# Kernel tuning notes

Hardware: AMD Instinct MI355X
Metric: run time of the kernel (lower is better)

Reference implementation:

```python
import jax, jax.numpy as jnp
import numpy as np

H = 16            # num_heads
D = 64            # head_output_size
DIM = 1024        # model dim (C)
R = 10            # lora rank
ATT_SCALE = D ** -0.5
LORA_SCALE = 1.0 / R   # lora_alpha(=1) / r


def setup_inputs() -> dict:
    key = jax.random.key(0)
    ks = jax.random.split(key, 14)
    B, N = 2, 2048
    s = 0.02
    x = jax.random.normal(ks[0], (B, N, DIM), jnp.float32)
    mask = jax.random.randint(ks[1], (B, N), 0, 2).astype(bool)
    return {
        "x": x,
        "mask": mask,
        "w_qkv": jax.random.normal(ks[2], (3 * H * D, DIM), jnp.float32) * s,
        "wq_base": jax.random.normal(ks[3], (H * D, DIM), jnp.float32) * s,
        "bq_base": jax.random.normal(ks[4], (H * D,), jnp.float32) * s,
        "wq_A": jax.random.normal(ks[5], (R, DIM), jnp.float32) * s,
        "wq_B": jax.random.normal(ks[6], (H * D, R), jnp.float32) * s,
        "wv_base": jax.random.normal(ks[7], (H * D, DIM), jnp.float32) * s,
        "bv_base": jax.random.normal(ks[8], (H * D,), jnp.float32) * s,
        "wv_A": jax.random.normal(ks[9], (R, DIM), jnp.float32) * s,
        "wv_B": jax.random.normal(ks[10], (H * D, R), jnp.float32) * s,
        "w_out": jax.random.normal(ks[11], (DIM, H * D), jnp.float32) * s,
        "b_out": jax.random.normal(ks[12], (DIM,), jnp.float32) * s,
    }


def _lora_linear(x, w_base, b_base, A, Bm):
    # lora.Linear (unmerged): base linear + scaled low-rank path
    return x @ w_base.T + b_base + ((x @ A.T) @ Bm.T) * LORA_SCALE


def reference(x, mask, w_qkv, wq_base, bq_base, wq_A, wq_B,
              wv_base, bv_base, wv_A, wv_B, w_out, b_out):
    B, N, C = x.shape
    # fused qkv projection -> (3, B, H, N, D)
    qkv = (x @ w_qkv.T).reshape(B, N, 3, H, D).transpose(2, 0, 3, 1, 4)
    q, k, v = qkv[0], qkv[1], qkv[2]
    # LoRA-modified q and v, reshaped to (B, H, N, D)
    q_lora = _lora_linear(x, wq_base, bq_base, wq_A, wq_B).reshape(B, N, H, D).transpose(0, 2, 1, 3)
    v_lora = _lora_linear(x, wv_base, bv_base, wv_A, wv_B).reshape(B, N, H, D).transpose(0, 2, 1, 3)
    q = q + q_lora
    v = v + v_lora
    # attention scores (B, H, N, N)
    attn = jnp.einsum('bhnd,bhmd->bhnm', q, k) * ATT_SCALE
    # 2D key-padding mask branch: mask[:, None, None, :]
    attn = jnp.where(mask[:, None, None, :], attn, -jnp.inf)
    attn = jax.nn.softmax(attn, axis=-1)
    out = jnp.einsum('bhnm,bhmd->bhnd', attn, v)
    out = out.transpose(0, 2, 1, 3).reshape(B, N, H * D)  # b h n d -> b n (h d)
    return out @ w_out.T + b_out
```

## Files before the change

kernel.cpp:

```cpp
#include <hip/hip_runtime.h>

typedef unsigned short u16;
typedef unsigned int u32;
typedef __attribute__((ext_vector_type(2))) unsigned int u32x2;
typedef __attribute__((ext_vector_type(4))) unsigned int u32x4;
typedef __attribute__((ext_vector_type(4))) unsigned short u16x4;
typedef __attribute__((ext_vector_type(8))) unsigned short u16x8;
typedef __attribute__((ext_vector_type(8))) short short8;
typedef __attribute__((ext_vector_type(4))) float f32x4;
typedef __attribute__((ext_vector_type(16))) float f32x16;

#define NHEAD 16
#define HDIM 64
#define SEQ 2048
#define MODELD 1024
#define MROWS 4096
#define QKVCOLS 3072
#define QSCALE 0.18033688011112042f

#define WAITVM(N) asm volatile("s_waitcnt vmcnt(" #N ")" ::: "memory")

__device__ __forceinline__ u16 f2bf(float f) {
  union { float f; unsigned u; } v; v.f = f;
  unsigned r = v.u + 0x7FFFu + ((v.u >> 16) & 1u);
  return (u16)(r >> 16);
}

__device__ __forceinline__ u32 cvtpk(float lo, float hi) {
  u32 r;
  asm("v_cvt_pk_bf16_f32 %0, %1, %2" : "=v"(r) : "v"(lo), "v"(hi));
  return r;
}

__device__ __forceinline__ void pl32(u32& a, u32& b) {
  asm("v_permlane32_swap_b32 %0, %1" : "+v"(a), "+v"(b));
}

__device__ __forceinline__ void gload_lds16(const void* g, void* l) {
  __builtin_amdgcn_global_load_lds((const __attribute__((address_space(1))) void*)g,
                                   (__attribute__((address_space(3))) void*)l, 16, 0, 0);
}


__global__ void prep_cast(const float* __restrict__ in, u16* __restrict__ outb) {
  int i = blockIdx.x * 256 + threadIdx.x;
  float4 v = *(const float4*)(in + (size_t)i * 4);
  u16x4 o = {f2bf(v.x), f2bf(v.y), f2bf(v.z), f2bf(v.w)};
  *(u16x4*)(outb + (size_t)i * 4) = o;
}

__global__ void prep_mask(const unsigned int* __restrict__ mraw, float* __restrict__ mf) {
  __shared__ int flag;
  const int tid = threadIdx.x;
  if (tid == 0) flag = 0;
  __syncthreads();
  if (mraw[tid] > 1u) flag = 1;
  __syncthreads();
  const int is_bytes = flag;
  const unsigned char* bp = (const unsigned char*)mraw;
#pragma unroll
  for (int j = 0; j < 4; ++j) {
    unsigned v = is_bytes ? (unsigned)bp[tid * 4 + j] : mraw[tid * 4 + j];
    mf[tid * 4 + j] = v ? 0.f : -1e30f;
  }
}

__global__ void prep_w(const float* __restrict__ wqkv,
                       const float* __restrict__ wqb, const float* __restrict__ bq,
                       const float* __restrict__ wqA, const float* __restrict__ wqB,
                       const float* __restrict__ wvb, const float* __restrict__ bv,
                       const float* __restrict__ wvA, const float* __restrict__ wvB,
                       u16* __restrict__ wcomb, float* __restrict__ biasc) {
  const int c = blockIdx.x;
  const int t = c >> 10, hd = c & 1023;
  const int k0 = threadIdx.x * 4;
  float4 w = *(const float4*)(wqkv + (size_t)c * MODELD + k0);
  float a0 = w.x, a1 = w.y, a2 = w.z, a3 = w.w;
  if (t != 1) {
    const float* base = (t == 0 ? wqb : wvb) + (size_t)hd * MODELD + k0;
    const float* A = (t == 0 ? wqA : wvA);
    const float* Bm = (t == 0 ? wqB : wvB) + hd * 10;
    float4 bsv = *(const float4*)base;
    a0 += bsv.x; a1 += bsv.y; a2 += bsv.z; a3 += bsv.w;
#pragma unroll
    for (int j = 0; j < 10; ++j) {
      float bj = Bm[j] * 0.1f;
      float4 av = *(const float4*)(A + (size_t)j * MODELD + k0);
      a0 += bj * av.x; a1 += bj * av.y; a2 += bj * av.z; a3 += bj * av.w;
    }
    if (t == 0) { a0 *= QSCALE; a1 *= QSCALE; a2 *= QSCALE; a3 *= QSCALE; }
  }
  u16x4 o = {f2bf(a0), f2bf(a1), f2bf(a2), f2bf(a3)};
  *(u16x4*)(wcomb + (size_t)c * MODELD + k0) = o;
  if (threadIdx.x == 0)
    biasc[c] = (t == 0) ? QSCALE * bq[hd] : ((t == 2) ? bv[hd] : 0.f);
}

template<int MODE>
__global__ __launch_bounds__(256) void gemm128(const u16* __restrict__ A, const u16* __restrict__ W,
                                               const float* __restrict__ bias,
                                               u16* __restrict__ oq, u16* __restrict__ ok, u16* __restrict__ ov,
                                               float* __restrict__ of) {
  __shared__ __align__(16) char lds[32768];
  const int tid = threadIdx.x;
  const int lane = tid & 63;
  const int wid = tid >> 6;
  const int wr = wid >> 1, wc = wid & 1;
  const int m0 = blockIdx.y << 7;
  const int n0 = blockIdx.x << 7;
  const int K = MODELD;

  f32x4 acc[4][4] = {};

  const int so = wid * 1024 + (lane << 4);
  for (int kt = 0; kt < K; kt += 64) {
#pragma unroll
    for (int c = 0; c < 4; ++c) {
      const int o = c * 4096 + so;
      const int row = o >> 7;
      const int colb = (o & 127) ^ ((row & 7) << 4);
      gload_lds16((const char*)(A + (size_t)(m0 + row) * K + kt) + colb, lds + (c * 4096 + wid * 1024));
      gload_lds16((const char*)(W + (size_t)(n0 + row) * K + kt) + colb, lds + (16384 + c * 4096 + wid * 1024));
    }
    __syncthreads();
#pragma unroll
    for (int ks = 0; ks < 2; ++ks) {
      short8 av[4], bv[4];
#pragma unroll
      for (int i = 0; i < 4; ++i) {
        const int arow = wr * 64 + i * 16 + (lane & 15);
        const int off = (ks * 64 + ((lane >> 4) << 4)) ^ ((lane & 7) << 4);
        av[i] = *(const short8*)(lds + (arow << 7) + off);
        const int brow = wc * 64 + i * 16 + (lane & 15);
        bv[i] = *(const short8*)(lds + 16384 + (brow << 7) + off);
      }
#pragma unroll
      for (int i = 0; i < 4; ++i)
#pragma unroll
        for (int j = 0; j < 4; ++j)
          acc[i][j] = __builtin_amdgcn_mfma_f32_16x16x32_bf16(av[i], bv[j], acc[i][j], 0, 0, 0);
    }
    __syncthreads();
  }

  if (MODE == 0) {
#pragma unroll
    for (int j = 0; j < 4; ++j) {
      const int col = n0 + wc * 64 + j * 16 + (lane & 15);
      const int tsel = col >> 10;
      const int hd = col & 1023;
      const int hh = hd >> 6, d = hd & 63;
      const float bs = bias[col];
#pragma unroll
      for (int i = 0; i < 4; ++i) {
        const int rowb = m0 + wr * 64 + i * 16 + ((lane >> 4) << 2);
#pragma unroll
        for (int r = 0; r < 4; ++r) {
          const int row = rowb + r;
          const int b = row >> 11, kv = row & 2047;
          const int bh = b * NHEAD + hh;
          const u16 val = f2bf(acc[i][j][r] + bs);
          if (tsel == 0) {
            oq[((size_t)bh * SEQ + kv) * HDIM + d] = val;
          } else if (tsel == 1) {
            ok[((size_t)(bh * 32 + (kv >> 6))) * 4096 +
               (size_t)(((((kv >> 5) & 1) << 2) + (d >> 4)) * 512) +
               (size_t)((((kv & 31) + (((d >> 3) & 1) << 5)) << 3) + (d & 7))] = val;
          } else {
            ov[((size_t)(bh * 32 + (kv >> 6))) * 4096 +
               (size_t)((((d >> 5) << 2) + ((kv >> 4) & 3)) * 512) +
               (size_t)((((d & 31) + (((kv >> 3) & 1) << 5)) << 3) + (kv & 7))] = val;
          }
        }
      }
    }
  } else {
#pragma unroll
    for (int j = 0; j < 4; ++j) {
      const int col = n0 + wc * 64 + j * 16 + (lane & 15);
      const float bs = bias[col];
#pragma unroll
      for (int i = 0; i < 4; ++i) {
        const int rowb = m0 + wr * 64 + i * 16 + ((lane >> 4) << 2);
#pragma unroll
        for (int r = 0; r < 4; ++r)
          of[(size_t)(rowb + r) * MODELD + col] = acc[i][j][r] + bs;
      }
    }
  }
}

__global__ __launch_bounds__(256) void flash_attn(const u16* __restrict__ q, const u16* __restrict__ kfr,
                                                  const u16* __restrict__ vfr, const float* __restrict__ maskf,
                                                  u16* __restrict__ attnout) {
  __shared__ __align__(16) char lds[73728];
  const int tid = threadIdx.x;
  const int lane = tid & 63, wid = tid >> 6;
  const int qi = lane & 31, h = lane >> 5;
  const int bid = blockIdx.x;
  const int bh = (bid & 7) * 4 + (bid >> 7);
  const int q0 = ((bid >> 3) & 15) * 128;
  const int b = bh >> 4, hh = bh & 15;

  const int token = q0 + wid * 32 + qi;
  short8 qf[4];
  {
    const u16* qp = q + ((size_t)bh * SEQ + token) * HDIM;
#pragma unroll
    for (int ks = 0; ks < 4; ++ks) qf[ks] = *(const short8*)(qp + ks * 16 + h * 8);
  }

  {
    const char* ms = (const char*)(maskf + b * SEQ);
    gload_lds16(ms + tid * 16, lds + 65536 + tid * 16);
    gload_lds16(ms + 4096 + tid * 16, lds + 65536 + 4096 + tid * 16);
  }

  const int so = tid << 4;
  const char* kg = (const char*)kfr + ((size_t)bh * 32) * 8192;
  const char* vg = (const char*)vfr + ((size_t)bh * 32) * 8192;
  auto stage = [&](int t) {
    char* kd = lds + ((t & 3) << 14);
    const char* ks = kg + (size_t)t * 8192;
    const char* vs = vg + (size_t)t * 8192;
    gload_lds16(ks + so, kd + so);
    gload_lds16(ks + 4096 + so, kd + 4096 + so);
    gload_lds16(vs + so, kd + 8192 + so);
    gload_lds16(vs + 4096 + so, kd + 12288 + so);
  };
  stage(0); stage(1); stage(2);

  f32x16 o0 = {}, o1 = {};
  f32x4 ps = {0.f, 0.f, 0.f, 0.f};

  for (int t = 0; t < 32; ++t) {
    if (t < 30)      { WAITVM(8); }
    else if (t == 30){ WAITVM(4); }
    else             { WAITVM(0); }
    asm volatile("s_barrier" ::: "memory");
    if (t <= 28) stage(t + 3);

    char* kb = lds + ((t & 3) << 14);
    char* vb = kb + 8192;
    const char* mrow = lds + 65536 + (t << 8);

    f32x16 s0 = {}, s1 = {};
    __builtin_amdgcn_s_setprio(1);
#pragma unroll
    for (int ks = 0; ks < 4; ++ks) {
      short8 ak0 = *(const short8*)(kb + (ks << 10) + (lane << 4));
      short8 ak1 = *(const short8*)(kb + 4096 + (ks << 10) + (lane << 4));
      s0 = __builtin_amdgcn_mfma_f32_32x32x16_bf16(ak0, qf[ks], s0, 0, 0, 0);
      s1 = __builtin_amdgcn_mfma_f32_32x32x16_bf16(ak1, qf[ks], s1, 0, 0, 0);
    }
    __builtin_amdgcn_s_setprio(0);

    u32 w[16];
#pragma unroll
    for (int blk = 0; blk < 2; ++blk) {
#pragma unroll
      for (int g = 0; g < 4; ++g) {
        f32x4 mk = *(const f32x4*)(mrow + blk * 128 + (g << 5) + (h << 4));
        float e0, e1, e2, e3;
        if (blk == 0) {
          e0 = exp2f(s0[4 * g + 0] + mk[0]); e1 = exp2f(s0[4 * g + 1] + mk[1]);
          e2 = exp2f(s0[4 * g + 2] + mk[2]); e3 = exp2f(s0[4 * g + 3] + mk[3]);
        } else {
          e0 = exp2f(s1[4 * g + 0] + mk[0]); e1 = exp2f(s1[4 * g + 1] + mk[1]);
          e2 = exp2f(s1[4 * g + 2] + mk[2]); e3 = exp2f(s1[4 * g + 3] + mk[3]);
        }
        ps[0] += e0; ps[1] += e1; ps[2] += e2; ps[3] += e3;
        w[blk * 8 + 2 * g] = cvtpk(e0, e1);
        w[blk * 8 + 2 * g + 1] = cvtpk(e2, e3);
      }
    }
    pl32(w[0], w[2]);  pl32(w[1], w[3]);
    pl32(w[4], w[6]);  pl32(w[5], w[7]);
    pl32(w[8], w[10]); pl32(w[9], w[11]);
    pl32(w[12], w[14]); pl32(w[13], w[15]);

    __builtin_amdgcn_s_setprio(1);
#pragma unroll
    for (int s = 0; s < 4; ++s) {
      u32x4 pw = {w[4 * s], w[4 * s + 1], w[4 * s + 2], w[4 * s + 3]};
      short8 pf = __builtin_bit_cast(short8, pw);
      short8 av0 = *(const short8*)(vb + (s << 10) + (lane << 4));
      short8 av1 = *(const short8*)(vb + 4096 + (s << 10) + (lane << 4));
      o0 = __builtin_amdgcn_mfma_f32_32x32x16_bf16(av0, pf, o0, 0, 0, 0);
      o1 = __builtin_amdgcn_mfma_f32_32x32x16_bf16(av1, pf, o1, 0, 0, 0);
    }
    __builtin_amdgcn_s_setprio(0);
  }

  float l = (ps[0] + ps[1]) + (ps[2] + ps[3]);
  l += __shfl_xor(l, 32);
  const float inv = 1.0f / l;

  u16* outp = attnout + ((size_t)(b * SEQ + token)) * MODELD + hh * HDIM;
#pragma unroll
  for (int dblk = 0; dblk < 2; ++dblk) {
#pragma unroll
    for (int g = 0; g < 4; ++g) {
      float v0, v1, v2, v3;
      if (dblk == 0) {
        v0 = o0[4 * g + 0]; v1 = o0[4 * g + 1]; v2 = o0[4 * g + 2]; v3 = o0[4 * g + 3];
      } else {
        v0 = o1[4 * g + 0]; v1 = o1[4 * g + 1]; v2 = o1[4 * g + 2]; v3 = o1[4 * g + 3];
      }
      u32x2 ow;
      ow[0] = cvtpk(v0 * inv, v1 * inv);
      ow[1] = cvtpk(v2 * inv, v3 * inv);
      *(u32x2*)(outp + dblk * 32 + g * 8 + h * 4) = ow;
    }
  }
}

extern "C" void kernel_launch(void* const* d_in, const int* in_sizes, int n_in,
                              void* d_out, int out_size, void* d_ws, size_t ws_size,
                              hipStream_t stream) {
  const float* x       = (const float*)d_in[0];
  const unsigned int* mask = (const unsigned int*)d_in[1];
  const float* w_qkv   = (const float*)d_in[2];
  const float* wq_base = (const float*)d_in[3];
  const float* bq      = (const float*)d_in[4];
  const float* wq_A    = (const float*)d_in[5];
  const float* wq_B    = (const float*)d_in[6];
  const float* wv_base = (const float*)d_in[7];
  const float* bv      = (const float*)d_in[8];
  const float* wv_A    = (const float*)d_in[9];
  const float* wv_B    = (const float*)d_in[10];
  const float* w_out   = (const float*)d_in[11];
  const float* b_out   = (const float*)d_in[12];
  float* out = (float*)d_out;

  char* ws = (char*)d_ws;
  u16* xb      = (u16*)(ws);
  u16* wcomb   = (u16*)(ws + 8388608);
  u16* woutb   = (u16*)(ws + 14680064);
  u16* qws     = (u16*)(ws + 16777216);
  u16* kws     = (u16*)(ws + 25165824);
  u16* vws     = (u16*)(ws + 33554432);
  float* biasc = (float*)(ws + 50331648);
  float* maskf = (float*)(ws + 50343936);
  u16* attnout = xb;

  prep_cast<<<4096, 256, 0, stream>>>(x, xb);
  prep_cast<<<1024, 256, 0, stream>>>(w_out, woutb);
  prep_mask<<<1, 1024, 0, stream>>>(mask, maskf);
  prep_w<<<3072, 256, 0, stream>>>(w_qkv, wq_base, bq, wq_A, wq_B,
                                   wv_base, bv, wv_A, wv_B, wcomb, biasc);

  gemm128<0><<<dim3(QKVCOLS / 128, MROWS / 128), 256, 0, stream>>>(
      xb, wcomb, biasc, qws, kws, vws, nullptr);

  flash_attn<<<512, 256, 0, stream>>>(qws, kws, vws, maskf, attnout);

  gemm128<1><<<dim3(MODELD / 128, MROWS / 128), 256, 0, stream>>>(
      attnout, woutb, b_out, nullptr, nullptr, nullptr, out);
}
```

Baseline: 162.1 us.

## Fold key-padding mask into QK MFMA as extra K column, shrink attention blocks

Encodes the key mask as an extra bf16 row in the K fragment layout, with -256 for masked keys. The query fragment gets a matching 1.0 entry, so an added fifth MFMA step applies the mask bias inside the score computation and the per-element mask loads and adds in the softmax are dropped. Attention blocks shrink from 256 to 128 threads (64 queries each, 1024 blocks). The pipeline goes from a 4-deep LDS ring with partial vmcnt waits to double buffering with a full wait every tile. This adds a mask_ext kernel, enlarges the K workspace, and costs 25% more QK MFMA work. The shallower prefetch may expose load latency, and a -256 bias may not fully zero masked keys unless scores are small.

```diff
diff --git a/kernel.cpp b/kernel.cpp
--- a/kernel.cpp
+++ b/kernel.cpp
@@ -49,7 +49,7 @@
   *(u16x4*)(outb + (size_t)i * 4) = o;
 }
 
-__global__ void prep_mask(const unsigned int* __restrict__ mraw, float* __restrict__ mf) {
+__global__ void prep_mask(const unsigned int* __restrict__ mraw, u16* __restrict__ mbf) {
   __shared__ int flag;
   const int tid = threadIdx.x;
   if (tid == 0) flag = 0;
@@ -58,11 +58,26 @@
   __syncthreads();
   const int is_bytes = flag;
   const unsigned char* bp = (const unsigned char*)mraw;
+  u16x4 o;
 #pragma unroll
   for (int j = 0; j < 4; ++j) {
     unsigned v = is_bytes ? (unsigned)bp[tid * 4 + j] : mraw[tid * 4 + j];
-    mf[tid * 4 + j] = v ? 0.f : -1e30f;
-  }
+    o[j] = v ? (u16)0x3F80 : (u16)0;
+  }
+  *(u16x4*)(mbf + tid * 4) = o;
+}
+
+__global__ void mask_ext(const u16* __restrict__ mbf, u16* __restrict__ kfr) {
+  const int tile = blockIdx.x, bh = blockIdx.y;
+  const int tid = threadIdx.x;
+  const int kvblk = tid >> 6, lane = tid & 63;
+  const int b = bh >> 4;
+  u16x8 o = {};
+  if (lane < 32) {
+    const int kv = tile * 64 + kvblk * 32 + lane;
+    o[0] = mbf[b * SEQ + kv] ? (u16)0 : (u16)0xC380;
+  }
+  *(u16x8*)(kfr + ((size_t)(bh * 32 + tile)) * 5120 + kvblk * 2560 + 2048 + lane * 8) = o;
 }
 
 __global__ void prep_w(const float* __restrict__ wqkv,
@@ -163,8 +178,9 @@
           if (tsel == 0) {
             oq[((size_t)bh * SEQ + kv) * HDIM + d] = val;
           } else if (tsel == 1) {
-            ok[((size_t)(bh * 32 + (kv >> 6))) * 4096 +
-               (size_t)(((((kv >> 5) & 1) << 2) + (d >> 4)) * 512) +
+            ok[((size_t)(bh * 32 + (kv >> 6))) * 5120 +
+               (size_t)((kv >> 5) & 1) * 2560 +
+               (size_t)(d >> 4) * 512 +
                (size_t)((((kv & 31) + (((d >> 3) & 1) << 5)) << 3) + (d & 7))] = val;
           } else {
             ov[((size_t)(bh * 32 + (kv >> 6))) * 4096 +
@@ -190,66 +206,60 @@
   }
 }
 
-__global__ __launch_bounds__(256) void flash_attn(const u16* __restrict__ q, const u16* __restrict__ kfr,
-                                                  const u16* __restrict__ vfr, const float* __restrict__ maskf,
+__global__ __launch_bounds__(128) void flash_attn(const u16* __restrict__ q, const u16* __restrict__ kfr,
+                                                  const u16* __restrict__ vfr,
                                                   u16* __restrict__ attnout) {
-  __shared__ __align__(16) char lds[73728];
+  __shared__ __align__(16) char lds[36864];
   const int tid = threadIdx.x;
   const int lane = tid & 63, wid = tid >> 6;
   const int qi = lane & 31, h = lane >> 5;
   const int bid = blockIdx.x;
-  const int bh = (bid & 7) * 4 + (bid >> 7);
-  const int q0 = ((bid >> 3) & 15) * 128;
+  const int xcd = bid & 7, rest = bid >> 3;
+  const int bh = xcd * 4 + (rest >> 5);
+  const int q0 = (rest & 31) << 6;
   const int b = bh >> 4, hh = bh & 15;
 
   const int token = q0 + wid * 32 + qi;
-  short8 qf[4];
+  short8 qf[5];
   {
     const u16* qp = q + ((size_t)bh * SEQ + token) * HDIM;
 #pragma unroll
     for (int ks = 0; ks < 4; ++ks) qf[ks] = *(const short8*)(qp + ks * 16 + h * 8);
-  }
-
-  {
-    const char* ms = (const char*)(maskf + b * SEQ);
-    gload_lds16(ms + tid * 16, lds + 65536 + tid * 16);
-    gload_lds16(ms + 4096 + tid * 16, lds + 65536 + 4096 + tid * 16);
-  }
-
+    qf[4] = short8{};
+    if (h == 0) qf[4][0] = (short)0x3F80;
+  }
+
+  const char* kg = (const char*)kfr + (size_t)bh * 32 * 10240;
+  const char* vg = (const char*)vfr + (size_t)bh * 32 * 8192;
   const int so = tid << 4;
-  const char* kg = (const char*)kfr + ((size_t)bh * 32) * 8192;
-  const char* vg = (const char*)vfr + ((size_t)bh * 32) * 8192;
-  auto stage = [&](int t) {
-    char* kd = lds + ((t & 3) << 14);
-    const char* ks = kg + (size_t)t * 8192;
+  auto stage = [&](int buf, int t) {
+    char* dst = lds + buf * 18432;
+    const char* ks = kg + (size_t)t * 10240;
     const char* vs = vg + (size_t)t * 8192;
-    gload_lds16(ks + so, kd + so);
-    gload_lds16(ks + 4096 + so, kd + 4096 + so);
-    gload_lds16(vs + so, kd + 8192 + so);
-    gload_lds16(vs + 4096 + so, kd + 12288 + so);
+#pragma unroll
+    for (int i = 0; i < 5; ++i) gload_lds16(ks + i * 2048 + so, dst + i * 2048 + so);
+#pragma unroll
+    for (int i = 0; i < 4; ++i) gload_lds16(vs + i * 2048 + so, dst + 10240 + i * 2048 + so);
   };
-  stage(0); stage(1); stage(2);
+  stage(0, 0);
 
   f32x16 o0 = {}, o1 = {};
   f32x4 ps = {0.f, 0.f, 0.f, 0.f};
 
   for (int t = 0; t < 32; ++t) {
-    if (t < 30)      { WAITVM(8); }
-    else if (t == 30){ WAITVM(4); }
-    else             { WAITVM(0); }
+    WAITVM(0);
     asm volatile("s_barrier" ::: "memory");
-    if (t <= 28) stage(t + 3);
-
-    char* kb = lds + ((t & 3) << 14);
-    char* vb = kb + 8192;
-    const char* mrow = lds + 65536 + (t << 8);
+    if (t < 31) stage((t + 1) & 1, t + 1);
+
+    char* kb = lds + (t & 1) * 18432;
+    char* vb = kb + 10240;
 
     f32x16 s0 = {}, s1 = {};
     __builtin_amdgcn_s_setprio(1);
 #pragma unroll
-    for (int ks = 0; ks < 4; ++ks) {
+    for (int ks = 0; ks < 5; ++ks) {
       short8 ak0 = *(const short8*)(kb + (ks << 10) + (lane << 4));
-      short8 ak1 = *(const short8*)(kb + 4096 + (ks << 10) + (lane << 4));
+      short8 ak1 = *(const short8*)(kb + 5120 + (ks << 10) + (lane << 4));
       s0 = __builtin_amdgcn_mfma_f32_32x32x16_bf16(ak0, qf[ks], s0, 0, 0, 0);
       s1 = __builtin_amdgcn_mfma_f32_32x32x16_bf16(ak1, qf[ks], s1, 0, 0, 0);
     }
@@ -260,14 +270,13 @@
     for (int blk = 0; blk < 2; ++blk) {
 #pragma unroll
       for (int g = 0; g < 4; ++g) {
-        f32x4 mk = *(const f32x4*)(mrow + blk * 128 + (g << 5) + (h << 4));
         float e0, e1, e2, e3;
         if (blk == 0) {
-          e0 = exp2f(s0[4 * g + 0] + mk[0]); e1 = exp2f(s0[4 * g + 1] + mk[1]);
-          e2 = exp2f(s0[4 * g + 2] + mk[2]); e3 = exp2f(s0[4 * g + 3] + mk[3]);
+          e0 = exp2f(s0[4 * g + 0]); e1 = exp2f(s0[4 * g + 1]);
+          e2 = exp2f(s0[4 * g + 2]); e3 = exp2f(s0[4 * g + 3]);
         } else {
-          e0 = exp2f(s1[4 * g + 0] + mk[0]); e1 = exp2f(s1[4 * g + 1] + mk[1]);
-          e2 = exp2f(s1[4 * g + 2] + mk[2]); e3 = exp2f(s1[4 * g + 3] + mk[3]);
+          e0 = exp2f(s1[4 * g + 0]); e1 = exp2f(s1[4 * g + 1]);
+          e2 = exp2f(s1[4 * g + 2]); e3 = exp2f(s1[4 * g + 3]);
         }
         ps[0] += e0; ps[1] += e1; ps[2] += e2; ps[3] += e3;
         w[blk * 8 + 2 * g] = cvtpk(e0, e1);
@@ -339,21 +348,22 @@
   u16* woutb   = (u16*)(ws + 14680064);
   u16* qws     = (u16*)(ws + 16777216);
   u16* kws     = (u16*)(ws + 25165824);
-  u16* vws     = (u16*)(ws + 33554432);
+  u16* vws     = (u16*)(ws + 35651584);
   float* biasc = (float*)(ws + 50331648);
-  float* maskf = (float*)(ws + 50343936);
+  u16* mbf     = (u16*)(ws + 50343936);
   u16* attnout = xb;
 
   prep_cast<<<4096, 256, 0, stream>>>(x, xb);
   prep_cast<<<1024, 256, 0, stream>>>(w_out, woutb);
-  prep_mask<<<1, 1024, 0, stream>>>(mask, maskf);
+  prep_mask<<<1, 1024, 0, stream>>>(mask, mbf);
+  mask_ext<<<dim3(32, 32), 128, 0, stream>>>(mbf, kws);
   prep_w<<<3072, 256, 0, stream>>>(w_qkv, wq_base, bq, wq_A, wq_B,
                                    wv_base, bv, wv_A, wv_B, wcomb, biasc);
 
   gemm128<0><<<dim3(QKVCOLS / 128, MROWS / 128), 256, 0, stream>>>(
       xb, wcomb, biasc, qws, kws, vws, nullptr);
 
-  flash_attn<<<512, 256, 0, stream>>>(qws, kws, vws, maskf, attnout);
+  flash_attn<<<1024, 128, 0, stream>>>(qws, kws, vws, attnout);
 
   gemm128<1><<<dim3(MODELD / 128, MROWS / 128), 256, 0, stream>>>(
       attnout, woutb, b_out, nullptr, nullptr, nullptr, out);
```

New measurement: 165.4 us (median of 2 runs). 2.0% more time.

## Load K/V straight to registers in single-wave attention, fold mask into MFMA

Applied to the files above, without the earlier changes.

The flash-attention kernel changes from 256-thread blocks that stage K/V tiles through LDS with barriers to single-wave blocks (2048 of them). Each wave loads K/V fragments straight from global memory into registers and prefetches the next tile. The key-padding mask becomes a bf16 bias that an extra MFMA adds into the scores (a ones column in Q), so the mask add before exp2 goes away and exp2 uses the raw hardware builtin. This removes LDS traffic and barriers, but each wave now reads K/V from global/L2 on its own with no sharing across waves, and register pressure rises.

```diff
diff --git a/kernel.cpp b/kernel.cpp
--- a/kernel.cpp
+++ b/kernel.cpp
@@ -18,8 +18,6 @@
 #define QKVCOLS 3072
 #define QSCALE 0.18033688011112042f
 
-#define WAITVM(N) asm volatile("s_waitcnt vmcnt(" #N ")" ::: "memory")
-
 __device__ __forceinline__ u16 f2bf(float f) {
   union { float f; unsigned u; } v; v.f = f;
   unsigned r = v.u + 0x7FFFu + ((v.u >> 16) & 1u);
@@ -49,7 +47,7 @@
   *(u16x4*)(outb + (size_t)i * 4) = o;
 }
 
-__global__ void prep_mask(const unsigned int* __restrict__ mraw, float* __restrict__ mf) {
+__global__ void prep_mask(const unsigned int* __restrict__ mraw, u16* __restrict__ mbf) {
   __shared__ int flag;
   const int tid = threadIdx.x;
   if (tid == 0) flag = 0;
@@ -58,11 +56,13 @@
   __syncthreads();
   const int is_bytes = flag;
   const unsigned char* bp = (const unsigned char*)mraw;
+  u16x4 o;
 #pragma unroll
   for (int j = 0; j < 4; ++j) {
     unsigned v = is_bytes ? (unsigned)bp[tid * 4 + j] : mraw[tid * 4 + j];
-    mf[tid * 4 + j] = v ? 0.f : -1e30f;
-  }
+    o[j] = v ? (u16)0 : (u16)0xC380;
+  }
+  *(u16x4*)(mbf + tid * 4) = o;
 }
 
 __global__ void prep_w(const float* __restrict__ wqkv,
@@ -190,88 +190,91 @@
   }
 }
 
-__global__ __launch_bounds__(256) void flash_attn(const u16* __restrict__ q, const u16* __restrict__ kfr,
-                                                  const u16* __restrict__ vfr, const float* __restrict__ maskf,
-                                                  u16* __restrict__ attnout) {
-  __shared__ __align__(16) char lds[73728];
-  const int tid = threadIdx.x;
-  const int lane = tid & 63, wid = tid >> 6;
+__global__ __launch_bounds__(64, 2) void flash_attn(const u16* __restrict__ q, const u16* __restrict__ kfr,
+                                                    const u16* __restrict__ vfr, const u16* __restrict__ mbf,
+                                                    u16* __restrict__ attnout) {
+  const int lane = threadIdx.x;
   const int qi = lane & 31, h = lane >> 5;
   const int bid = blockIdx.x;
-  const int bh = (bid & 7) * 4 + (bid >> 7);
-  const int q0 = ((bid >> 3) & 15) * 128;
+  const int xcd = bid & 7, rest = bid >> 3;
+  const int bh = xcd * 4 + (rest >> 6);
+  const int q0 = (rest & 63) << 5;
   const int b = bh >> 4, hh = bh & 15;
 
-  const int token = q0 + wid * 32 + qi;
-  short8 qf[4];
+  const int token = q0 + qi;
+  short8 qf[4], qf4 = {};
   {
     const u16* qp = q + ((size_t)bh * SEQ + token) * HDIM;
 #pragma unroll
     for (int ks = 0; ks < 4; ++ks) qf[ks] = *(const short8*)(qp + ks * 16 + h * 8);
-  }
-
-  {
-    const char* ms = (const char*)(maskf + b * SEQ);
-    gload_lds16(ms + tid * 16, lds + 65536 + tid * 16);
-    gload_lds16(ms + 4096 + tid * 16, lds + 65536 + 4096 + tid * 16);
-  }
-
-  const int so = tid << 4;
-  const char* kg = (const char*)kfr + ((size_t)bh * 32) * 8192;
-  const char* vg = (const char*)vfr + ((size_t)bh * 32) * 8192;
-  auto stage = [&](int t) {
-    char* kd = lds + ((t & 3) << 14);
-    const char* ks = kg + (size_t)t * 8192;
-    const char* vs = vg + (size_t)t * 8192;
-    gload_lds16(ks + so, kd + so);
-    gload_lds16(ks + 4096 + so, kd + 4096 + so);
-    gload_lds16(vs + so, kd + 8192 + so);
-    gload_lds16(vs + 4096 + so, kd + 12288 + so);
-  };
-  stage(0); stage(1); stage(2);
+    if (h == 0) qf4[0] = (short)0x3F80;
+  }
+
+  const u16* kg = kfr + (size_t)bh * 32 * 4096;
+  const u16* vg = vfr + (size_t)bh * 32 * 4096;
+  const u16* mrow = mbf + b * SEQ;
+  const int lo = lane << 3;
+
+  short8 kS[8], vS[8];
+  u16 m0v, m1v;
 
   f32x16 o0 = {}, o1 = {};
   f32x4 ps = {0.f, 0.f, 0.f, 0.f};
 
+  {
+    const u16* kt = kg;
+    const u16* vt = vg;
+#pragma unroll
+    for (int i = 0; i < 8; ++i) kS[i] = *(const short8*)(kt + i * 512 + lo);
+#pragma unroll
+    for (int i = 0; i < 8; ++i) vS[i] = *(const short8*)(vt + i * 512 + lo);
+    m0v = mrow[qi];
+    m1v = mrow[32 + qi];
+  }
+
   for (int t = 0; t < 32; ++t) {
-    if (t < 30)      { WAITVM(8); }
-    else if (t == 30){ WAITVM(4); }
-    else             { WAITVM(0); }
-    asm volatile("s_barrier" ::: "memory");
-    if (t <= 28) stage(t + 3);
-
-    char* kb = lds + ((t & 3) << 14);
-    char* vb = kb + 8192;
-    const char* mrow = lds + 65536 + (t << 8);
+    short8 e0 = {}, e1 = {};
+    if (h == 0) { e0[0] = (short)m0v; e1[0] = (short)m1v; }
 
     f32x16 s0 = {}, s1 = {};
     __builtin_amdgcn_s_setprio(1);
 #pragma unroll
     for (int ks = 0; ks < 4; ++ks) {
-      short8 ak0 = *(const short8*)(kb + (ks << 10) + (lane << 4));
-      short8 ak1 = *(const short8*)(kb + 4096 + (ks << 10) + (lane << 4));
-      s0 = __builtin_amdgcn_mfma_f32_32x32x16_bf16(ak0, qf[ks], s0, 0, 0, 0);
-      s1 = __builtin_amdgcn_mfma_f32_32x32x16_bf16(ak1, qf[ks], s1, 0, 0, 0);
-    }
+      s0 = __builtin_amdgcn_mfma_f32_32x32x16_bf16(kS[ks], qf[ks], s0, 0, 0, 0);
+      s1 = __builtin_amdgcn_mfma_f32_32x32x16_bf16(kS[4 + ks], qf[ks], s1, 0, 0, 0);
+    }
+    s0 = __builtin_amdgcn_mfma_f32_32x32x16_bf16(e0, qf4, s0, 0, 0, 0);
+    s1 = __builtin_amdgcn_mfma_f32_32x32x16_bf16(e1, qf4, s1, 0, 0, 0);
     __builtin_amdgcn_s_setprio(0);
 
+    if (t < 31) {
+      const u16* kt = kg + (size_t)(t + 1) * 4096;
+#pragma unroll
+      for (int i = 0; i < 8; ++i) kS[i] = *(const short8*)(kt + i * 512 + lo);
+      m0v = mrow[(t + 1) * 64 + qi];
+      m1v = mrow[(t + 1) * 64 + 32 + qi];
+    }
+
     u32 w[16];
 #pragma unroll
     for (int blk = 0; blk < 2; ++blk) {
 #pragma unroll
       for (int g = 0; g < 4; ++g) {
-        f32x4 mk = *(const f32x4*)(mrow + blk * 128 + (g << 5) + (h << 4));
-        float e0, e1, e2, e3;
+        float e0f, e1f, e2f, e3f;
         if (blk == 0) {
-          e0 = exp2f(s0[4 * g + 0] + mk[0]); e1 = exp2f(s0[4 * g + 1] + mk[1]);
-          e2 = exp2f(s0[4 * g + 2] + mk[2]); e3 = exp2f(s0[4 * g + 3] + mk[3]);
+          e0f = __builtin_amdgcn_exp2f(s0[4 * g + 0]);
+          e1f = __builtin_amdgcn_exp2f(s0[4 * g + 1]);
+          e2f = __builtin_amdgcn_exp2f(s0[4 * g + 2]);
+          e3f = __builtin_amdgcn_exp2f(s0[4 * g + 3]);
         } else {
-          e0 = exp2f(s1[4 * g + 0] + mk[0]); e1 = exp2f(s1[4 * g + 1] + mk[1]);
-          e2 = exp2f(s1[4 * g + 2] + mk[2]); e3 = exp2f(s1[4 * g + 3] + mk[3]);
+          e0f = __builtin_amdgcn_exp2f(s1[4 * g + 0]);
+          e1f = __builtin_amdgcn_exp2f(s1[4 * g + 1]);
+          e2f = __builtin_amdgcn_exp2f(s1[4 * g + 2]);
+          e3f = __builtin_amdgcn_exp2f(s1[4 * g + 3]);
         }
-        ps[0] += e0; ps[1] += e1; ps[2] += e2; ps[3] += e3;
-        w[blk * 8 + 2 * g] = cvtpk(e0, e1);
-        w[blk * 8 + 2 * g + 1] = cvtpk(e2, e3);
+        ps[0] += e0f; ps[1] += e1f; ps[2] += e2f; ps[3] += e3f;
+        w[blk * 8 + 2 * g] = cvtpk(e0f, e1f);
+        w[blk * 8 + 2 * g + 1] = cvtpk(e2f, e3f);
       }
     }
     pl32(w[0], w[2]);  pl32(w[1], w[3]);
@@ -284,12 +287,16 @@
     for (int s = 0; s < 4; ++s) {
       u32x4 pw = {w[4 * s], w[4 * s + 1], w[4 * s + 2], w[4 * s + 3]};
       short8 pf = __builtin_bit_cast(short8, pw);
-      short8 av0 = *(const short8*)(vb + (s << 10) + (lane << 4));
-      short8 av1 = *(const short8*)(vb + 4096 + (s << 10) + (lane << 4));
-      o0 = __builtin_amdgcn_mfma_f32_32x32x16_bf16(av0, pf, o0, 0, 0, 0);
-      o1 = __builtin_amdgcn_mfma_f32_32x32x16_bf16(av1, pf, o1, 0, 0, 0);
+      o0 = __builtin_amdgcn_mfma_f32_32x32x16_bf16(vS[s], pf, o0, 0, 0, 0);
+      o1 = __builtin_amdgcn_mfma_f32_32x32x16_bf16(vS[4 + s], pf, o1, 0, 0, 0);
     }
     __builtin_amdgcn_s_setprio(0);
+
+    if (t < 31) {
+      const u16* vt = vg + (size_t)(t + 1) * 4096;
+#pragma unroll
+      for (int i = 0; i < 8; ++i) vS[i] = *(const short8*)(vt + i * 512 + lo);
+    }
   }
 
   float l = (ps[0] + ps[1]) + (ps[2] + ps[3]);
@@ -341,19 +348,19 @@
   u16* kws     = (u16*)(ws + 25165824);
   u16* vws     = (u16*)(ws + 33554432);
   float* biasc = (float*)(ws + 50331648);
-  float* maskf = (float*)(ws + 50343936);
+  u16* mbf     = (u16*)(ws + 50343936);
   u16* attnout = xb;
 
   prep_cast<<<4096, 256, 0, stream>>>(x, xb);
   prep_cast<<<1024, 256, 0, stream>>>(w_out, woutb);
-  prep_mask<<<1, 1024, 0, stream>>>(mask, maskf);
+  prep_mask<<<1, 1024, 0, stream>>>(mask, mbf);
   prep_w<<<3072, 256, 0, stream>>>(w_qkv, wq_base, bq, wq_A, wq_B,
                                    wv_base, bv, wv_A, wv_B, wcomb, biasc);
 
   gemm128<0><<<dim3(QKVCOLS / 128, MROWS / 128), 256, 0, stream>>>(
       xb, wcomb, biasc, qws, kws, vws, nullptr);
 
-  flash_attn<<<512, 256, 0, stream>>>(qws, kws, vws, maskf, attnout);
+  flash_attn<<<2048, 64, 0, stream>>>(qws, kws, vws, mbf, attnout);
 
   gemm128<1><<<dim3(MODELD / 128, MROWS / 128), 256, 0, stream>>>(
       attnout, woutb, b_out, nullptr, nullptr, nullptr, out);
```

Result: faster. 152.0 us (-6.2%).
